# Kernel tuning notes

Hardware: AMD Instinct MI355X
Metric: run time of the kernel (lower is better)

## Reference

```python
import jax, jax.numpy as jnp
import numpy as np

N_FP = 235336   # n_fingerprint
N_WORD = 7844   # n_word
D = 10          # embed / hidden dim (hard-coded in module)
K = 23          # conv kernel 2*11+1
PAD = 11
N_ATOMS = 4096
L_WORDS = 65536


def setup_inputs() -> dict:
    key = jax.random.key(0)
    ks = jax.random.split(key, 16)
    s = 0.1  # weight init scale
    return {
        "fingerprints": jax.random.randint(ks[0], (N_ATOMS,), 0, N_FP),
        # scale adjacency so x + A@hs stays O(1) over 3 layers
        "adjacency": jax.random.uniform(ks[1], (N_ATOMS, N_ATOMS), dtype=jnp.float32) * (1.0 / N_ATOMS),
        "words": jax.random.randint(ks[2], (L_WORDS,), 0, N_WORD),
        "embed_fp": jax.random.normal(ks[3], (N_FP, D), dtype=jnp.float32) * s,
        "embed_word": jax.random.normal(ks[4], (N_WORD, D), dtype=jnp.float32) * s,
        "W_gnn_w": jax.random.normal(ks[5], (3, D, D), dtype=jnp.float32) * s,
        "W_gnn_b": jax.random.normal(ks[6], (3, D), dtype=jnp.float32) * s,
        "W_cnn_w": jax.random.normal(ks[7], (3, 1, 1, K, K), dtype=jnp.float32) * (s / K),
        "W_cnn_b": jax.random.normal(ks[8], (3,), dtype=jnp.float32) * s,
        "W_att_w": jax.random.normal(ks[9], (D, D), dtype=jnp.float32) * s,
        "W_att_b": jax.random.normal(ks[10], (D,), dtype=jnp.float32) * s,
        "W_out_w": jax.random.normal(ks[11], (3, 2 * D, 2 * D), dtype=jnp.float32) * s,
        "W_out_b": jax.random.normal(ks[12], (3, 2 * D), dtype=jnp.float32) * s,
        "W_int_w": jax.random.normal(ks[13], (2, 2 * D), dtype=jnp.float32) * s,
        "W_int_b": jax.random.normal(ks[14], (2,), dtype=jnp.float32) * s,
    }


def reference(fingerprints, adjacency, words, embed_fp, embed_word,
              W_gnn_w, W_gnn_b, W_cnn_w, W_cnn_b, W_att_w, W_att_b,
              W_out_w, W_out_b, W_int_w, W_int_b):
    # ---- Compound vector with GNN ----
    xs = embed_fp[fingerprints]                       # [N, D]
    for i in range(3):                                # fixed 3 layers
        hs = jax.nn.relu(xs @ W_gnn_w[i].T + W_gnn_b[i])
        xs = xs + adjacency @ hs                      # dense message passing
    compound = jnp.mean(xs, axis=0, keepdims=True)    # [1, D]

    # ---- Protein vector with attention-CNN ----
    ws = embed_word[words]                            # [L, D]
    t = ws[None, None]                                # [1,1,L,D] NCHW
    for i in range(3):
        t = jax.nn.relu(
            jax.lax.conv_general_dilated(t, W_cnn_w[i], (1, 1),
                                          [(PAD, PAD), (PAD, PAD)])
            + W_cnn_b[i])
    xs_p = t[0, 0]                                    # [L, D]

    h = jax.nn.relu(compound @ W_att_w.T + W_att_b)   # [1, D]
    hs_p = jax.nn.relu(xs_p @ W_att_w.T + W_att_b)    # [L, D]
    weights = jnp.tanh(h @ hs_p.T)                    # [1, L]
    ys = weights.T * hs_p                             # [L, D]
    protein = jnp.mean(ys, axis=0, keepdims=True)     # [1, D]

    # ---- Fusion MLP ----
    cat = jnp.concatenate([compound, protein], axis=1)  # [1, 2D]
    for j in range(3):
        cat = jax.nn.relu(cat @ W_out_w[j].T + W_out_b[j])
    return cat @ W_int_w.T + W_int_b                  # [1, 2]
```

## Files before the change

### kernel.cpp

```cpp
#include <hip/hip_runtime.h>
#include <hip/hip_bf16.h>
#include <math.h>

#define N_ATOMS 4096
#define L_WORDS 65536
#define DD 10
#define HALO 11

__global__ __launch_bounds__(256) void gnn_embed(
    const int* __restrict__ fp, const float* __restrict__ embed_fp,
    const float* __restrict__ Wg0, const float* __restrict__ bg0,
    float* __restrict__ xs0, float* __restrict__ hsT0)
{
    int n = blockIdx.x * blockDim.x + threadIdx.x;
    if (n >= N_ATOMS) return;
    float x[DD];
    const float* e = embed_fp + (size_t)fp[n] * DD;
    #pragma unroll
    for (int d = 0; d < DD; ++d) { x[d] = e[d]; xs0[n * DD + d] = x[d]; }
    #pragma unroll
    for (int d = 0; d < DD; ++d) {
        float v = bg0[d];
        #pragma unroll
        for (int k = 0; k < DD; ++k) v += Wg0[d * DD + k] * x[k];
        hsT0[d * N_ATOMS + n] = fmaxf(v, 0.f);
    }
}

#define GP_BLOCK 256
#define GP_RPW 4
#define GP_ROWS_BLK 16
#define GP_QCOLS 1024
#define CONV_BLOCKS 256
#define CONV_BLOCK 256

__global__ __launch_bounds__(256, 4) void fused_layer(
    const float* __restrict__ A,
    const float* __restrict__ hsT_in,
    float* __restrict__ part,
    const float* __restrict__ tin,
    const int* __restrict__ words,
    const float* __restrict__ embed_word,
    const float* __restrict__ w,
    const float* __restrict__ bptr,
    float* __restrict__ tout)
{
    __shared__ float sh[DD * GP_QCOLS];
    const int tid = threadIdx.x;

    if (blockIdx.x < CONV_BLOCKS) {
        float* s = sh;
        const int l0 = blockIdx.x * CONV_BLOCK;

        for (int idx = tid; idx < (CONV_BLOCK + 2 * HALO) * DD; idx += CONV_BLOCK) {
            int rr = idx / DD, d = idx - rr * DD;
            int gr = l0 - HALO + rr;
            float v = 0.f;
            if (gr >= 0 && gr < L_WORDS) {
                if (tin) v = tin[(size_t)gr * DD + d];
                else     v = embed_word[(size_t)words[gr] * DD + d];
            }
            s[rr * 11 + d] = v;
        }
        __syncthreads();

        const float bias = *bptr;
        float acc[DD];
        #pragma unroll
        for (int d = 0; d < DD; ++d) acc[d] = bias;

        for (int i = 0; i < 23; ++i) {
            float row[DD];
            const float* sr = &s[(tid + i) * 11];
            #pragma unroll
            for (int c = 0; c < DD; ++c) row[c] = sr[c];
            #pragma unroll
            for (int d = 0; d < DD; ++d) {
                #pragma unroll
                for (int c = 0; c < DD; ++c)
                    acc[d] += row[c] * w[i * 23 + (c - d + 11)];
            }
        }
        const int l = l0 + tid;
        #pragma unroll
        for (int d = 0; d < DD; ++d)
            tout[(size_t)l * DD + d] = fmaxf(acc[d], 0.f);
    } else {
        const int b = blockIdx.x - CONV_BLOCKS;
        const int wave = tid >> 6, lane = tid & 63;
        const int q = b & 3, rg = b >> 2;
        const int qbase = q * GP_QCOLS;

        {
            const float4* src = (const float4*)(hsT_in + qbase);
            float4* dst = (float4*)sh;
            #pragma unroll
            for (int k = 0; k < DD; ++k)
                dst[k * 256 + tid] = src[k * (N_ATOMS / 4) + tid];
        }
        __syncthreads();

        const int r0 = rg * GP_ROWS_BLK + wave * GP_RPW;
        const float4* Ar[GP_RPW];
        #pragma unroll
        for (int r = 0; r < GP_RPW; ++r)
            Ar[r] = (const float4*)(A + (size_t)(r0 + r) * N_ATOMS + qbase);
        const float4* sh4 = (const float4*)sh;

        float acc[GP_RPW][DD];
        #pragma unroll
        for (int r = 0; r < GP_RPW; ++r)
            #pragma unroll
            for (int d = 0; d < DD; ++d) acc[r][d] = 0.f;

        #pragma unroll
        for (int it = 0; it < GP_QCOLS / 256; ++it) {
            const int cb = it * 64 + lane;
            float4 a[GP_RPW];
            #pragma unroll
            for (int r = 0; r < GP_RPW; ++r) a[r] = Ar[r][cb];
            #pragma unroll
            for (int d = 0; d < DD; ++d) {
                float4 h = sh4[d * 256 + cb];
                #pragma unroll
                for (int r = 0; r < GP_RPW; ++r) {
                    acc[r][d] += a[r].x * h.x;
                    acc[r][d] += a[r].y * h.y;
                    acc[r][d] += a[r].z * h.z;
                    acc[r][d] += a[r].w * h.w;
                }
            }
        }

        #pragma unroll
        for (int m = 32; m >= 1; m >>= 1) {
            #pragma unroll
            for (int r = 0; r < GP_RPW; ++r)
                #pragma unroll
                for (int d = 0; d < DD; ++d)
                    acc[r][d] += __shfl_xor(acc[r][d], m, 64);
        }

        if (lane == 0) {
            #pragma unroll
            for (int r = 0; r < GP_RPW; ++r)
                #pragma unroll
                for (int d = 0; d < DD; ++d)
                    part[((size_t)q * N_ATOMS + r0 + r) * DD + d] = acc[r][d];
        }
    }
}

__global__ __launch_bounds__(256) void gnn_combine(
    const float* __restrict__ xs_in,
    const float* __restrict__ part,
    float* __restrict__ xs_out,
    float* __restrict__ hsT_out,
    const float* __restrict__ Wg,
    const float* __restrict__ bg,
    float* __restrict__ comp_part)
{
    const int tid = threadIdx.x, wave = tid >> 6, lane = tid & 63;
    const int n = blockIdx.x * 256 + tid;

    float x[DD];
    #pragma unroll
    for (int d = 0; d < DD; ++d) {
        float v = xs_in[n * DD + d];
        #pragma unroll
        for (int q = 0; q < 4; ++q)
            v += part[((size_t)q * N_ATOMS + n) * DD + d];
        x[d] = v;
        xs_out[n * DD + d] = v;
    }
    if (hsT_out) {
        #pragma unroll
        for (int d = 0; d < DD; ++d) {
            float v = bg[d];
            #pragma unroll
            for (int k = 0; k < DD; ++k) v += Wg[d * DD + k] * x[k];
            hsT_out[(size_t)d * N_ATOMS + n] = fmaxf(v, 0.f);
        }
    }
    if (comp_part) {
        #pragma unroll
        for (int m = 32; m >= 1; m >>= 1) {
            #pragma unroll
            for (int d = 0; d < DD; ++d) x[d] += __shfl_xor(x[d], m, 64);
        }
        __shared__ float s[4][DD];
        if (lane == 0) {
            #pragma unroll
            for (int d = 0; d < DD; ++d) s[wave][d] = x[d];
        }
        __syncthreads();
        if (tid < DD)
            comp_part[blockIdx.x * DD + tid] =
                s[0][tid] + s[1][tid] + s[2][tid] + s[3][tid];
    }
}

__global__ __launch_bounds__(256) void reduce_comp(
    const float* __restrict__ part, int npart, float* __restrict__ comp)
{
    const int tid = threadIdx.x, wave = tid >> 6, lane = tid & 63;
    float v[DD];
    #pragma unroll
    for (int d = 0; d < DD; ++d) v[d] = 0.f;
    for (int p = tid; p < npart; p += 256) {
        #pragma unroll
        for (int d = 0; d < DD; ++d) v[d] += part[p * DD + d];
    }
    #pragma unroll
    for (int off = 32; off >= 1; off >>= 1) {
        #pragma unroll
        for (int d = 0; d < DD; ++d) v[d] += __shfl_down(v[d], off, 64);
    }
    __shared__ float s[4][DD];
    if (lane == 0) {
        #pragma unroll
        for (int d = 0; d < DD; ++d) s[wave][d] = v[d];
    }
    __syncthreads();
    if (tid < DD)
        comp[tid] = (s[0][tid] + s[1][tid] + s[2][tid] + s[3][tid]) * (1.f / N_ATOMS);
}

__global__ __launch_bounds__(1024) void attention_pool(
    const float* __restrict__ xs_p,
    const float* __restrict__ comp,
    const float* __restrict__ Wa, const float* __restrict__ ba,
    float* __restrict__ att_part)
{
    const int tid = threadIdx.x, wave = tid >> 6, lane = tid & 63;
    const int l = blockIdx.x * 1024 + tid;

    float h[DD];
    #pragma unroll
    for (int d = 0; d < DD; ++d) {
        float v = ba[d];
        #pragma unroll
        for (int k = 0; k < DD; ++k) v += Wa[d * DD + k] * comp[k];
        h[d] = fmaxf(v, 0.f);
    }

    float row[DD];
    #pragma unroll
    for (int d = 0; d < DD; ++d) row[d] = xs_p[(size_t)l * DD + d];

    float hp[DD], dotv = 0.f;
    #pragma unroll
    for (int d = 0; d < DD; ++d) {
        float v = ba[d];
        #pragma unroll
        for (int k = 0; k < DD; ++k) v += Wa[d * DD + k] * row[k];
        hp[d] = fmaxf(v, 0.f);
        dotv += h[d] * hp[d];
    }
    const float wgt = tanhf(dotv);

    float y[DD];
    #pragma unroll
    for (int d = 0; d < DD; ++d) y[d] = wgt * hp[d];

    #pragma unroll
    for (int off = 32; off >= 1; off >>= 1) {
        #pragma unroll
        for (int d = 0; d < DD; ++d) y[d] += __shfl_down(y[d], off, 64);
    }
    __shared__ float s[16][DD];
    if (lane == 0) {
        #pragma unroll
        for (int d = 0; d < DD; ++d) s[wave][d] = y[d];
    }
    __syncthreads();
    if (tid < DD) {
        float v = 0.f;
        #pragma unroll
        for (int wv = 0; wv < 16; ++wv) v += s[wv][tid];
        att_part[blockIdx.x * DD + tid] = v;
    }
}

__global__ __launch_bounds__(64) void final_mlp(
    const float* __restrict__ comp,
    const float* __restrict__ att_part,
    const float* __restrict__ Wo, const float* __restrict__ bo,
    const float* __restrict__ Wi, const float* __restrict__ bi,
    float* __restrict__ out)
{
    const int t = threadIdx.x;
    float a[DD];
    #pragma unroll
    for (int d = 0; d < DD; ++d) a[d] = att_part[t * DD + d];
    #pragma unroll
    for (int off = 32; off >= 1; off >>= 1) {
        #pragma unroll
        for (int d = 0; d < DD; ++d) a[d] += __shfl_down(a[d], off, 64);
    }

    __shared__ float cat[20];
    if (t < DD) cat[t] = comp[t];
    if (t == 0) {
        #pragma unroll
        for (int d = 0; d < DD; ++d) cat[DD + d] = a[d] * (1.f / L_WORDS);
    }
    __syncthreads();

    for (int j = 0; j < 3; ++j) {
        float v = 0.f;
        if (t < 20) {
            v = bo[j * 20 + t];
            for (int k = 0; k < 20; ++k) v += Wo[j * 400 + t * 20 + k] * cat[k];
        }
        __syncthreads();
        if (t < 20) cat[t] = fmaxf(v, 0.f);
        __syncthreads();
    }
    if (t < 2) {
        float v = bi[t];
        for (int k = 0; k < 20; ++k) v += Wi[t * 20 + k] * cat[k];
        out[t] = v;
    }
}

extern "C" void kernel_launch(void* const* d_in, const int* in_sizes, int n_in,
                              void* d_out, int out_size, void* d_ws, size_t ws_size,
                              hipStream_t stream)
{
    const int*   fp     = (const int*)d_in[0];
    const float* A      = (const float*)d_in[1];
    const int*   words  = (const int*)d_in[2];
    const float* emb_fp = (const float*)d_in[3];
    const float* emb_w  = (const float*)d_in[4];
    const float* Wg     = (const float*)d_in[5];
    const float* bg     = (const float*)d_in[6];
    const float* Wc     = (const float*)d_in[7];
    const float* bc     = (const float*)d_in[8];
    const float* Wa     = (const float*)d_in[9];
    const float* ba     = (const float*)d_in[10];
    const float* Wo     = (const float*)d_in[11];
    const float* bo     = (const float*)d_in[12];
    const float* Wi     = (const float*)d_in[13];
    const float* bi     = (const float*)d_in[14];
    float* out = (float*)d_out;
    float* ws  = (float*)d_ws;

    float* xs0  = ws;
    float* xs1  = ws + 40960;
    float* hsT0 = ws + 81920;
    float* hsT1 = ws + 122880;
    float* t0   = ws + 163840;
    float* t1   = ws + 163840 + 655360;
    float* comp = ws + 163840 + 2 * 655360;
    float* part = comp + 16;
    float* comp_part = part + 163840;
    float* att_part  = comp_part + 256;

    const int fused_grid = CONV_BLOCKS + (N_ATOMS / GP_ROWS_BLK) * 4;

    gnn_embed<<<N_ATOMS / 256, 256, 0, stream>>>(fp, emb_fp, Wg, bg, xs0, hsT0);

    fused_layer<<<fused_grid, 256, 0, stream>>>(
        A, hsT0, part, nullptr, words, emb_w, Wc, bc, t0);
    gnn_combine<<<N_ATOMS / 256, 256, 0, stream>>>(
        xs0, part, xs1, hsT1, Wg + 100, bg + 10, nullptr);

    fused_layer<<<fused_grid, 256, 0, stream>>>(
        A, hsT1, part, t0, nullptr, nullptr, Wc + 529, bc + 1, t1);
    gnn_combine<<<N_ATOMS / 256, 256, 0, stream>>>(
        xs1, part, xs0, hsT0, Wg + 200, bg + 20, nullptr);

    fused_layer<<<fused_grid, 256, 0, stream>>>(
        A, hsT0, part, t1, nullptr, nullptr, Wc + 1058, bc + 2, t0);
    gnn_combine<<<N_ATOMS / 256, 256, 0, stream>>>(
        xs0, part, xs1, nullptr, nullptr, nullptr, comp_part);
    reduce_comp<<<1, 256, 0, stream>>>(comp_part, 16, comp);

    attention_pool<<<L_WORDS / 1024, 1024, 0, stream>>>(t0, comp, Wa, ba, att_part);
    final_mlp<<<1, 64, 0, stream>>>(comp, att_part, Wo, bo, Wi, bi, out);
}
```

Before: 233.6 us.

## Fuse whole pipeline into one cooperative persistent kernel with grid syncs

Replaces the sequence of about eleven kernel launches (embed, three fused GNN+conv layers, combines, reductions, attention, MLP) with a single cooperatively launched persistent kernel of 768 blocks that separates phases with grid-wide syncs. The adjacency matmul is also re-split into eight 512-column slices, which halves the shared memory per block so three blocks fit per CU, and the combine step sums eight partials. This is meant to remove launch gaps and tail effects between the many small dependent stages. In exchange it adds eight grid barriers, and it falls back to the old multi-kernel path if the cooperative launch fails.

Result: slower. 909.5 us (+289.4%).

```diff
diff --git a/kernel.cpp b/kernel.cpp
--- a/kernel.cpp
+++ b/kernel.cpp
@@ -1,49 +1,395 @@
 #include <hip/hip_runtime.h>
 #include <hip/hip_bf16.h>
+#include <hip/hip_cooperative_groups.h>
 #include <math.h>
+
+namespace cg = cooperative_groups;
 
 #define N_ATOMS 4096
 #define L_WORDS 65536
 #define DD 10
 #define HALO 11
 
-__global__ __launch_bounds__(256) void gnn_embed(
-    const int* __restrict__ fp, const float* __restrict__ embed_fp,
-    const float* __restrict__ Wg0, const float* __restrict__ bg0,
-    float* __restrict__ xs0, float* __restrict__ hsT0)
-{
-    int n = blockIdx.x * blockDim.x + threadIdx.x;
-    if (n >= N_ATOMS) return;
-    float x[DD];
-    const float* e = embed_fp + (size_t)fp[n] * DD;
-    #pragma unroll
-    for (int d = 0; d < DD; ++d) { x[d] = e[d]; xs0[n * DD + d] = x[d]; }
-    #pragma unroll
-    for (int d = 0; d < DD; ++d) {
-        float v = bg0[d];
-        #pragma unroll
-        for (int k = 0; k < DD; ++k) v += Wg0[d * DD + k] * x[k];
-        hsT0[d * N_ATOMS + n] = fmaxf(v, 0.f);
-    }
-}
-
-#define GP_BLOCK 256
+#define MG_GRID 768
+#define MG_BLOCK 256
+#define MG_QC 512
+#define MG_NQ 8
+#define MG_RPB 16
+#define MG_NRG (N_ATOMS / MG_RPB)
+#define MG_NGNN (MG_NQ * MG_NRG)
+#define MG_NCONV 256
+#define MG_NU (MG_NCONV + MG_NGNN)
+
+struct MegaArgs {
+    const int* fp; const float* A; const int* words;
+    const float* emb_fp; const float* emb_w;
+    const float* Wg; const float* bg; const float* Wc; const float* bc;
+    const float* Wa; const float* ba; const float* Wo; const float* bo;
+    const float* Wi; const float* bi;
+    float* out;
+    float* xs0; float* xs1; float* hsT0; float* hsT1;
+    float* ta; float* tb; float* part; float* comp_part; float* att_part;
+};
+
+__device__ __forceinline__ void mg_gnn_unit(
+    int g, const float* __restrict__ A, const float* __restrict__ hsT_in,
+    float* __restrict__ part, float* sh)
+{
+    const int tid = threadIdx.x, wave = tid >> 6, lane = tid & 63;
+    const int q = g & (MG_NQ - 1), rg = g >> 3;
+    const int qb4 = q * (MG_QC / 4);
+
+    {
+        const float4* src = (const float4*)hsT_in;
+        float4* dst = (float4*)sh;
+        #pragma unroll
+        for (int k = 0; k < 5; ++k) {
+            int idx = k * 256 + tid;
+            int row = idx >> 7, col = idx & 127;
+            dst[row * 128 + col] = src[(size_t)row * (N_ATOMS / 4) + qb4 + col];
+        }
+    }
+    __syncthreads();
+
+    const int r0 = rg * MG_RPB + wave * 4;
+    const float4* Ar = (const float4*)(A + (size_t)r0 * N_ATOMS) + qb4;
+    const float4* sh4 = (const float4*)sh;
+
+    float acc[4][DD];
+    #pragma unroll
+    for (int r = 0; r < 4; ++r)
+        #pragma unroll
+        for (int d = 0; d < DD; ++d) acc[r][d] = 0.f;
+
+    #pragma unroll
+    for (int it = 0; it < 2; ++it) {
+        const int cb = it * 64 + lane;
+        float4 a0 = Ar[cb];
+        float4 a1 = Ar[1024 + cb];
+        float4 a2 = Ar[2048 + cb];
+        float4 a3 = Ar[3072 + cb];
+        #pragma unroll
+        for (int d = 0; d < DD; ++d) {
+            float4 h = sh4[d * 128 + cb];
+            acc[0][d] += a0.x*h.x + a0.y*h.y + a0.z*h.z + a0.w*h.w;
+            acc[1][d] += a1.x*h.x + a1.y*h.y + a1.z*h.z + a1.w*h.w;
+            acc[2][d] += a2.x*h.x + a2.y*h.y + a2.z*h.z + a2.w*h.w;
+            acc[3][d] += a3.x*h.x + a3.y*h.y + a3.z*h.z + a3.w*h.w;
+        }
+    }
+
+    #pragma unroll
+    for (int m = 32; m >= 1; m >>= 1) {
+        #pragma unroll
+        for (int r = 0; r < 4; ++r)
+            #pragma unroll
+            for (int d = 0; d < DD; ++d)
+                acc[r][d] += __shfl_xor(acc[r][d], m, 64);
+    }
+    if (lane == 0) {
+        #pragma unroll
+        for (int r = 0; r < 4; ++r)
+            #pragma unroll
+            for (int d = 0; d < DD; ++d)
+                part[((size_t)q * N_ATOMS + r0 + r) * DD + d] = acc[r][d];
+    }
+    __syncthreads();
+}
+
+__device__ __forceinline__ void mg_conv_unit(
+    int c, const float* __restrict__ tin, const int* __restrict__ words,
+    const float* __restrict__ emb_w, const float* __restrict__ w,
+    const float* __restrict__ bptr, float* __restrict__ tout, float* sh)
+{
+    const int tid = threadIdx.x;
+    const int l0 = c * 256;
+
+    for (int idx = tid; idx < (256 + 2 * HALO) * DD; idx += 256) {
+        int rr = idx / DD, d = idx - rr * DD;
+        int gr = l0 - HALO + rr;
+        float v = 0.f;
+        if (gr >= 0 && gr < L_WORDS) {
+            if (tin) v = tin[(size_t)gr * DD + d];
+            else     v = emb_w[(size_t)words[gr] * DD + d];
+        }
+        sh[rr * 11 + d] = v;
+    }
+    __syncthreads();
+
+    const float bias = *bptr;
+    float acc[DD];
+    #pragma unroll
+    for (int d = 0; d < DD; ++d) acc[d] = bias;
+
+    for (int i = 0; i < 23; ++i) {
+        float row[DD];
+        const float* sr = &sh[(tid + i) * 11];
+        #pragma unroll
+        for (int cc = 0; cc < DD; ++cc) row[cc] = sr[cc];
+        #pragma unroll
+        for (int d = 0; d < DD; ++d) {
+            #pragma unroll
+            for (int cc = 0; cc < DD; ++cc)
+                acc[d] += row[cc] * w[i * 23 + (cc - d + 11)];
+        }
+    }
+    const int l = l0 + tid;
+    #pragma unroll
+    for (int d = 0; d < DD; ++d)
+        tout[(size_t)l * DD + d] = fmaxf(acc[d], 0.f);
+    __syncthreads();
+}
+
+__device__ __forceinline__ void mg_phaseA(
+    int layer, const float* A, const float* hsT_in, float* part,
+    const float* tin, const int* words, const float* emb_w,
+    const float* Wc, const float* bc, float* tout, float* sh)
+{
+    for (int u = blockIdx.x; u < MG_NU; u += MG_GRID) {
+        if (u < MG_NCONV)
+            mg_conv_unit(u, tin, words, emb_w, Wc + 529 * layer, bc + layer,
+                         tout, sh);
+        else
+            mg_gnn_unit(u - MG_NCONV, A, hsT_in, part, sh);
+    }
+}
+
+__device__ __forceinline__ void mg_combine(
+    const float* xs_in, const float* part, float* xs_out, float* hsT_out,
+    const float* Wg, const float* bg, float* comp_part, float* sh)
+{
+    if (blockIdx.x < 16) {
+        const int tid = threadIdx.x, wave = tid >> 6, lane = tid & 63;
+        const int n = blockIdx.x * 256 + tid;
+        float x[DD];
+        #pragma unroll
+        for (int d = 0; d < DD; ++d) {
+            float v = xs_in[n * DD + d];
+            #pragma unroll
+            for (int q = 0; q < MG_NQ; ++q)
+                v += part[((size_t)q * N_ATOMS + n) * DD + d];
+            x[d] = v;
+        }
+        if (xs_out) {
+            #pragma unroll
+            for (int d = 0; d < DD; ++d) xs_out[n * DD + d] = x[d];
+        }
+        if (hsT_out) {
+            #pragma unroll
+            for (int d = 0; d < DD; ++d) {
+                float v = bg[d];
+                #pragma unroll
+                for (int k = 0; k < DD; ++k) v += Wg[d * DD + k] * x[k];
+                hsT_out[(size_t)d * N_ATOMS + n] = fmaxf(v, 0.f);
+            }
+        }
+        if (comp_part) {
+            #pragma unroll
+            for (int m = 32; m >= 1; m >>= 1) {
+                #pragma unroll
+                for (int d = 0; d < DD; ++d) x[d] += __shfl_xor(x[d], m, 64);
+            }
+            if (lane == 0) {
+                #pragma unroll
+                for (int d = 0; d < DD; ++d) sh[wave * DD + d] = x[d];
+            }
+            __syncthreads();
+            if (tid < DD)
+                comp_part[blockIdx.x * DD + tid] =
+                    sh[tid] + sh[DD + tid] + sh[2 * DD + tid] + sh[3 * DD + tid];
+        }
+    }
+}
+
+__device__ __forceinline__ void mg_att(
+    const float* xs_p, const float* comp_part,
+    const float* Wa, const float* ba, float* att_part, float* sh)
+{
+    if (blockIdx.x < 256) {
+        const int tid = threadIdx.x, wave = tid >> 6, lane = tid & 63;
+        if (tid < DD) {
+            float c = 0.f;
+            #pragma unroll
+            for (int p = 0; p < 16; ++p) c += comp_part[p * DD + tid];
+            sh[tid] = c * (1.f / N_ATOMS);
+        }
+        __syncthreads();
+        float compv[DD];
+        #pragma unroll
+        for (int d = 0; d < DD; ++d) compv[d] = sh[d];
+
+        float h[DD];
+        #pragma unroll
+        for (int d = 0; d < DD; ++d) {
+            float v = ba[d];
+            #pragma unroll
+            for (int k = 0; k < DD; ++k) v += Wa[d * DD + k] * compv[k];
+            h[d] = fmaxf(v, 0.f);
+        }
+
+        const int l = blockIdx.x * 256 + tid;
+        float row[DD];
+        #pragma unroll
+        for (int d = 0; d < DD; ++d) row[d] = xs_p[(size_t)l * DD + d];
+
+        float hp[DD], dotv = 0.f;
+        #pragma unroll
+        for (int d = 0; d < DD; ++d) {
+            float v = ba[d];
+            #pragma unroll
+            for (int k = 0; k < DD; ++k) v += Wa[d * DD + k] * row[k];
+            hp[d] = fmaxf(v, 0.f);
+            dotv += h[d] * hp[d];
+        }
+        const float wgt = tanhf(dotv);
+
+        float y[DD];
+        #pragma unroll
+        for (int d = 0; d < DD; ++d) y[d] = wgt * hp[d];
+        #pragma unroll
+        for (int m = 32; m >= 1; m >>= 1) {
+            #pragma unroll
+            for (int d = 0; d < DD; ++d) y[d] += __shfl_xor(y[d], m, 64);
+        }
+        __syncthreads();
+        if (lane == 0) {
+            #pragma unroll
+            for (int d = 0; d < DD; ++d) sh[wave * DD + d] = y[d];
+        }
+        __syncthreads();
+        if (tid < DD)
+            att_part[blockIdx.x * DD + tid] =
+                sh[tid] + sh[DD + tid] + sh[2 * DD + tid] + sh[3 * DD + tid];
+    }
+}
+
+__device__ __forceinline__ void mg_fin(
+    const float* att_part, const float* comp_part,
+    const float* Wo, const float* bo, const float* Wi, const float* bi,
+    float* out, float* sh)
+{
+    if (blockIdx.x == 0) {
+        const int tid = threadIdx.x, wave = tid >> 6, lane = tid & 63;
+        float v[DD];
+        #pragma unroll
+        for (int d = 0; d < DD; ++d) v[d] = att_part[tid * DD + d];
+        #pragma unroll
+        for (int m = 32; m >= 1; m >>= 1) {
+            #pragma unroll
+            for (int d = 0; d < DD; ++d) v[d] += __shfl_xor(v[d], m, 64);
+        }
+        if (lane == 0) {
+            #pragma unroll
+            for (int d = 0; d < DD; ++d) sh[32 + wave * DD + d] = v[d];
+        }
+        __syncthreads();
+        if (tid < DD) {
+            float c = 0.f;
+            #pragma unroll
+            for (int p = 0; p < 16; ++p) c += comp_part[p * DD + tid];
+            sh[tid] = c * (1.f / N_ATOMS);
+            float pr = sh[32 + tid] + sh[32 + DD + tid]
+                     + sh[32 + 2 * DD + tid] + sh[32 + 3 * DD + tid];
+            sh[DD + tid] = pr * (1.f / L_WORDS);
+        }
+        __syncthreads();
+        for (int j = 0; j < 3; ++j) {
+            float vv = 0.f;
+            if (tid < 20) {
+                vv = bo[j * 20 + tid];
+                for (int k = 0; k < 20; ++k)
+                    vv += Wo[j * 400 + tid * 20 + k] * sh[k];
+            }
+            __syncthreads();
+            if (tid < 20) sh[tid] = fmaxf(vv, 0.f);
+            __syncthreads();
+        }
+        if (tid < 2) {
+            float vv = bi[tid];
+            for (int k = 0; k < 20; ++k) vv += Wi[tid * 20 + k] * sh[k];
+            out[tid] = vv;
+        }
+    }
+}
+
+__global__ __launch_bounds__(MG_BLOCK, 3) void mega(MegaArgs a)
+{
+    __shared__ float sh[DD * MG_QC];
+    cg::grid_group grid = cg::this_grid();
+    const int tid = threadIdx.x;
+
+    if (blockIdx.x < 16) {
+        const int n = blockIdx.x * 256 + tid;
+        float x[DD];
+        const float* e = a.emb_fp + (size_t)a.fp[n] * DD;
+        #pragma unroll
+        for (int d = 0; d < DD; ++d) { x[d] = e[d]; a.xs0[n * DD + d] = x[d]; }
+        #pragma unroll
+        for (int d = 0; d < DD; ++d) {
+            float v = a.bg[d];
+            #pragma unroll
+            for (int k = 0; k < DD; ++k) v += a.Wg[d * DD + k] * x[k];
+            a.hsT0[(size_t)d * N_ATOMS + n] = fmaxf(v, 0.f);
+        }
+    }
+    grid.sync();
+
+    mg_phaseA(0, a.A, a.hsT0, a.part, nullptr, a.words, a.emb_w, a.Wc, a.bc,
+              a.ta, sh);
+    grid.sync();
+    mg_combine(a.xs0, a.part, a.xs1, a.hsT1, a.Wg + 100, a.bg + 10, nullptr, sh);
+    grid.sync();
+
+    mg_phaseA(1, a.A, a.hsT1, a.part, a.ta, a.words, a.emb_w, a.Wc, a.bc,
+              a.tb, sh);
+    grid.sync();
+    mg_combine(a.xs1, a.part, a.xs0, a.hsT0, a.Wg + 200, a.bg + 20, nullptr, sh);
+    grid.sync();
+
+    mg_phaseA(2, a.A, a.hsT0, a.part, a.tb, a.words, a.emb_w, a.Wc, a.bc,
+              a.ta, sh);
+    grid.sync();
+    mg_combine(a.xs0, a.part, nullptr, nullptr, nullptr, nullptr,
+               a.comp_part, sh);
+    grid.sync();
+
+    mg_att(a.ta, a.comp_part, a.Wa, a.ba, a.att_part, sh);
+    grid.sync();
+    mg_fin(a.att_part, a.comp_part, a.Wo, a.bo, a.Wi, a.bi, a.out, sh);
+}
+
 #define GP_RPW 4
 #define GP_ROWS_BLK 16
 #define GP_QCOLS 1024
 #define CONV_BLOCKS 256
 #define CONV_BLOCK 256
 
+__global__ __launch_bounds__(256) void gnn_embed(
+    const int* __restrict__ fp, const float* __restrict__ embed_fp,
+    const float* __restrict__ Wg0, const float* __restrict__ bg0,
+    float* __restrict__ xs0, float* __restrict__ hsT0)
+{
+    int n = blockIdx.x * blockDim.x + threadIdx.x;
+    if (n >= N_ATOMS) return;
+    float x[DD];
+    const float* e = embed_fp + (size_t)fp[n] * DD;
+    #pragma unroll
+    for (int d = 0; d < DD; ++d) { x[d] = e[d]; xs0[n * DD + d] = x[d]; }
+    #pragma unroll
+    for (int d = 0; d < DD; ++d) {
+        float v = bg0[d];
+        #pragma unroll
+        for (int k = 0; k < DD; ++k) v += Wg0[d * DD + k] * x[k];
+        hsT0[d * N_ATOMS + n] = fmaxf(v, 0.f);
+    }
+}
+
 __global__ __launch_bounds__(256, 4) void fused_layer(
-    const float* __restrict__ A,
-    const float* __restrict__ hsT_in,
+    const float* __restrict__ A, const float* __restrict__ hsT_in,
     float* __restrict__ part,
-    const float* __restrict__ tin,
-    const int* __restrict__ words,
-    const float* __restrict__ embed_word,
-    const float* __restrict__ w,
-    const float* __restrict__ bptr,
-    float* __restrict__ tout)
+    const float* __restrict__ tin, const int* __restrict__ words,
+    const float* __restrict__ embed_word, const float* __restrict__ w,
+    const float* __restrict__ bptr, float* __restrict__ tout)
 {
     __shared__ float sh[DD * GP_QCOLS];
     const int tid = threadIdx.x;
@@ -51,7 +397,6 @@
     if (blockIdx.x < CONV_BLOCKS) {
         float* s = sh;
         const int l0 = blockIdx.x * CONV_BLOCK;
-
         for (int idx = tid; idx < (CONV_BLOCK + 2 * HALO) * DD; idx += CONV_BLOCK) {
             int rr = idx / DD, d = idx - rr * DD;
             int gr = l0 - HALO + rr;
@@ -63,12 +408,10 @@
             s[rr * 11 + d] = v;
         }
         __syncthreads();
-
         const float bias = *bptr;
         float acc[DD];
         #pragma unroll
         for (int d = 0; d < DD; ++d) acc[d] = bias;
-
         for (int i = 0; i < 23; ++i) {
             float row[DD];
             const float* sr = &s[(tid + i) * 11];
@@ -90,7 +433,6 @@
         const int wave = tid >> 6, lane = tid & 63;
         const int q = b & 3, rg = b >> 2;
         const int qbase = q * GP_QCOLS;
-
         {
             const float4* src = (const float4*)(hsT_in + qbase);
             float4* dst = (float4*)sh;
@@ -99,39 +441,35 @@
                 dst[k * 256 + tid] = src[k * (N_ATOMS / 4) + tid];
         }
         __syncthreads();
-
         const int r0 = rg * GP_ROWS_BLK + wave * GP_RPW;
         const float4* Ar[GP_RPW];
         #pragma unroll
         for (int r = 0; r < GP_RPW; ++r)
             Ar[r] = (const float4*)(A + (size_t)(r0 + r) * N_ATOMS + qbase);
         const float4* sh4 = (const float4*)sh;
-
         float acc[GP_RPW][DD];
         #pragma unroll
         for (int r = 0; r < GP_RPW; ++r)
             #pragma unroll
             for (int d = 0; d < DD; ++d) acc[r][d] = 0.f;
-
         #pragma unroll
         for (int it = 0; it < GP_QCOLS / 256; ++it) {
             const int cb = it * 64 + lane;
-            float4 a[GP_RPW];
-            #pragma unroll
-            for (int r = 0; r < GP_RPW; ++r) a[r] = Ar[r][cb];
+            float4 av[GP_RPW];
+            #pragma unroll
+            for (int r = 0; r < GP_RPW; ++r) av[r] = Ar[r][cb];
             #pragma unroll
             for (int d = 0; d < DD; ++d) {
                 float4 h = sh4[d * 256 + cb];
                 #pragma unroll
                 for (int r = 0; r < GP_RPW; ++r) {
-                    acc[r][d] += a[r].x * h.x;
-                    acc[r][d] += a[r].y * h.y;
-                    acc[r][d] += a[r].z * h.z;
-                    acc[r][d] += a[r].w * h.w;
+                    acc[r][d] += av[r].x * h.x;
+                    acc[r][d] += av[r].y * h.y;
+                    acc[r][d] += av[r].z * h.z;
+                    acc[r][d] += av[r].w * h.w;
                 }
             }
         }
-
         #pragma unroll
         for (int m = 32; m >= 1; m >>= 1) {
             #pragma unroll
@@ -140,7 +478,6 @@
                 for (int d = 0; d < DD; ++d)
                     acc[r][d] += __shfl_xor(acc[r][d], m, 64);
         }
-
         if (lane == 0) {
             #pragma unroll
             for (int r = 0; r < GP_RPW; ++r)
@@ -152,17 +489,13 @@
 }
 
 __global__ __launch_bounds__(256) void gnn_combine(
-    const float* __restrict__ xs_in,
-    const float* __restrict__ part,
-    float* __restrict__ xs_out,
-    float* __restrict__ hsT_out,
-    const float* __restrict__ Wg,
-    const float* __restrict__ bg,
+    const float* __restrict__ xs_in, const float* __restrict__ part,
+    float* __restrict__ xs_out, float* __restrict__ hsT_out,
+    const float* __restrict__ Wg, const float* __restrict__ bg,
     float* __restrict__ comp_part)
 {
     const int tid = threadIdx.x, wave = tid >> 6, lane = tid & 63;
     const int n = blockIdx.x * 256 + tid;
-
     float x[DD];
     #pragma unroll
     for (int d = 0; d < DD; ++d) {
@@ -227,14 +560,12 @@
 }
 
 __global__ __launch_bounds__(1024) void attention_pool(
-    const float* __restrict__ xs_p,
-    const float* __restrict__ comp,
+    const float* __restrict__ xs_p, const float* __restrict__ comp,
     const float* __restrict__ Wa, const float* __restrict__ ba,
     float* __restrict__ att_part)
 {
     const int tid = threadIdx.x, wave = tid >> 6, lane = tid & 63;
     const int l = blockIdx.x * 1024 + tid;
-
     float h[DD];
     #pragma unroll
     for (int d = 0; d < DD; ++d) {
@@ -243,11 +574,9 @@
         for (int k = 0; k < DD; ++k) v += Wa[d * DD + k] * comp[k];
         h[d] = fmaxf(v, 0.f);
     }
-
     float row[DD];
     #pragma unroll
     for (int d = 0; d < DD; ++d) row[d] = xs_p[(size_t)l * DD + d];
-
     float hp[DD], dotv = 0.f;
     #pragma unroll
     for (int d = 0; d < DD; ++d) {
@@ -258,11 +587,9 @@
         dotv += h[d] * hp[d];
     }
     const float wgt = tanhf(dotv);
-
     float y[DD];
     #pragma unroll
     for (int d = 0; d < DD; ++d) y[d] = wgt * hp[d];
-
     #pragma unroll
     for (int off = 32; off >= 1; off >>= 1) {
         #pragma unroll
@@ -283,8 +610,7 @@
 }
 
 __global__ __launch_bounds__(64) void final_mlp(
-    const float* __restrict__ comp,
-    const float* __restrict__ att_part,
+    const float* __restrict__ comp, const float* __restrict__ att_part,
     const float* __restrict__ Wo, const float* __restrict__ bo,
     const float* __restrict__ Wi, const float* __restrict__ bi,
     float* __restrict__ out)
@@ -298,7 +624,6 @@
         #pragma unroll
         for (int d = 0; d < DD; ++d) a[d] += __shfl_down(a[d], off, 64);
     }
-
     __shared__ float cat[20];
     if (t < DD) cat[t] = comp[t];
     if (t == 0) {
@@ -306,7 +631,6 @@
         for (int d = 0; d < DD; ++d) cat[DD + d] = a[d] * (1.f / L_WORDS);
     }
     __syncthreads();
-
     for (int j = 0; j < 3; ++j) {
         float v = 0.f;
         if (t < 20) {
@@ -350,33 +674,38 @@
     float* xs1  = ws + 40960;
     float* hsT0 = ws + 81920;
     float* hsT1 = ws + 122880;
-    float* t0   = ws + 163840;
-    float* t1   = ws + 163840 + 655360;
-    float* comp = ws + 163840 + 2 * 655360;
-    float* part = comp + 16;
-    float* comp_part = part + 163840;
-    float* att_part  = comp_part + 256;
-
-    const int fused_grid = CONV_BLOCKS + (N_ATOMS / GP_ROWS_BLK) * 4;
-
-    gnn_embed<<<N_ATOMS / 256, 256, 0, stream>>>(fp, emb_fp, Wg, bg, xs0, hsT0);
-
-    fused_layer<<<fused_grid, 256, 0, stream>>>(
-        A, hsT0, part, nullptr, words, emb_w, Wc, bc, t0);
-    gnn_combine<<<N_ATOMS / 256, 256, 0, stream>>>(
-        xs0, part, xs1, hsT1, Wg + 100, bg + 10, nullptr);
-
-    fused_layer<<<fused_grid, 256, 0, stream>>>(
-        A, hsT1, part, t0, nullptr, nullptr, Wc + 529, bc + 1, t1);
-    gnn_combine<<<N_ATOMS / 256, 256, 0, stream>>>(
-        xs1, part, xs0, hsT0, Wg + 200, bg + 20, nullptr);
-
-    fused_layer<<<fused_grid, 256, 0, stream>>>(
-        A, hsT0, part, t1, nullptr, nullptr, Wc + 1058, bc + 2, t0);
-    gnn_combine<<<N_ATOMS / 256, 256, 0, stream>>>(
-        xs0, part, xs1, nullptr, nullptr, nullptr, comp_part);
-    reduce_comp<<<1, 256, 0, stream>>>(comp_part, 16, comp);
-
-    attention_pool<<<L_WORDS / 1024, 1024, 0, stream>>>(t0, comp, Wa, ba, att_part);
-    final_mlp<<<1, 64, 0, stream>>>(comp, att_part, Wo, bo, Wi, bi, out);
-}
+    float* ta   = ws + 163840;
+    float* tb   = ws + 819200;
+    float* part = ws + 1474560;
+    float* comp_part = ws + 1802240;
+    float* att_part  = ws + 1802496;
+    float* comp      = ws + 1805056;
+
+    MegaArgs ma = { fp, A, words, emb_fp, emb_w, Wg, bg, Wc, bc,
+                    Wa, ba, Wo, bo, Wi, bi, out,
+                    xs0, xs1, hsT0, hsT1, ta, tb, part, comp_part, att_part };
+    void* kp[1] = { &ma };
+    hipError_t err = hipLaunchCooperativeKernel(
+        (void*)mega, dim3(MG_GRID), dim3(MG_BLOCK), kp, 0, stream);
+
+    if (err != hipSuccess) {
+        (void)hipGetLastError();
+        const int fused_grid = CONV_BLOCKS + (N_ATOMS / GP_ROWS_BLK) * 4;
+        gnn_embed<<<N_ATOMS / 256, 256, 0, stream>>>(fp, emb_fp, Wg, bg, xs0, hsT0);
+        fused_layer<<<fused_grid, 256, 0, stream>>>(
+            A, hsT0, part, nullptr, words, emb_w, Wc, bc, ta);
+        gnn_combine<<<N_ATOMS / 256, 256, 0, stream>>>(
+            xs0, part, xs1, hsT1, Wg + 100, bg + 10, nullptr);
+        fused_layer<<<fused_grid, 256, 0, stream>>>(
+            A, hsT1, part, ta, nullptr, nullptr, Wc + 529, bc + 1, tb);
+        gnn_combine<<<N_ATOMS / 256, 256, 0, stream>>>(
+            xs1, part, xs0, hsT0, Wg + 200, bg + 20, nullptr);
+        fused_layer<<<fused_grid, 256, 0, stream>>>(
+            A, hsT0, part, tb, nullptr, nullptr, Wc + 1058, bc + 2, ta);
+        gnn_combine<<<N_ATOMS / 256, 256, 0, stream>>>(
+            xs0, part, xs1, nullptr, nullptr, nullptr, comp_part);
+        reduce_comp<<<1, 256, 0, stream>>>(comp_part, 16, comp);
+        attention_pool<<<L_WORDS / 1024, 1024, 0, stream>>>(ta, comp, Wa, ba, att_part);
+        final_mlp<<<1, 64, 0, stream>>>(comp, att_part, Wo, bo, Wi, bi, out);
+    }
+}
```

## Fuse GNN combine and final reductions into producer kernels via last-block atomics

Applied to the files above, without the earlier changes.

Removes the separate gnn_combine, reduce_comp and final_mlp launches. The last of the four column-quarter blocks for each row group (detected with an atomic counter) does the combine, the next-layer hidden projection and the compound partial sums, and a second counter lets the last block produce the compound mean. The attention kernel likewise uses a last-block counter to run the final MLP. Counters are zeroed inside the embed kernel. This cuts launch overhead and inter-kernel gaps in exchange for extra threadfences and atomics, plus a serial tail in the last block.

New measurement: 769.9 us. +229.6%, slower.

```diff
diff --git a/kernel.cpp b/kernel.cpp
--- a/kernel.cpp
+++ b/kernel.cpp
@@ -7,51 +7,59 @@
 #define DD 10
 #define HALO 11
 
-__global__ __launch_bounds__(256) void gnn_embed(
-    const int* __restrict__ fp, const float* __restrict__ embed_fp,
-    const float* __restrict__ Wg0, const float* __restrict__ bg0,
-    float* __restrict__ xs0, float* __restrict__ hsT0)
-{
-    int n = blockIdx.x * blockDim.x + threadIdx.x;
-    if (n >= N_ATOMS) return;
-    float x[DD];
-    const float* e = embed_fp + (size_t)fp[n] * DD;
-    #pragma unroll
-    for (int d = 0; d < DD; ++d) { x[d] = e[d]; xs0[n * DD + d] = x[d]; }
-    #pragma unroll
-    for (int d = 0; d < DD; ++d) {
-        float v = bg0[d];
-        #pragma unroll
-        for (int k = 0; k < DD; ++k) v += Wg0[d * DD + k] * x[k];
-        hsT0[d * N_ATOMS + n] = fmaxf(v, 0.f);
-    }
-}
-
-#define GP_BLOCK 256
 #define GP_RPW 4
 #define GP_ROWS_BLK 16
 #define GP_QCOLS 1024
 #define CONV_BLOCKS 256
 #define CONV_BLOCK 256
+#define N_RG (N_ATOMS / GP_ROWS_BLK)
+
+__global__ __launch_bounds__(256) void gnn_embed(
+    const int* __restrict__ fp, const float* __restrict__ embed_fp,
+    const float* __restrict__ Wg0, const float* __restrict__ bg0,
+    float* __restrict__ xs0, float* __restrict__ hsT0,
+    int* __restrict__ cnts)
+{
+    const int tid = threadIdx.x;
+    if (blockIdx.x == 0) {
+        for (int i = tid; i < 3 * N_RG + 2; i += 256) cnts[i] = 0;
+    }
+    int n = blockIdx.x * blockDim.x + tid;
+    if (n >= N_ATOMS) return;
+    float x[DD];
+    const float* e = embed_fp + (size_t)fp[n] * DD;
+    #pragma unroll
+    for (int d = 0; d < DD; ++d) { x[d] = e[d]; xs0[n * DD + d] = x[d]; }
+    #pragma unroll
+    for (int d = 0; d < DD; ++d) {
+        float v = bg0[d];
+        #pragma unroll
+        for (int k = 0; k < DD; ++k) v += Wg0[d * DD + k] * x[k];
+        hsT0[d * N_ATOMS + n] = fmaxf(v, 0.f);
+    }
+}
 
 __global__ __launch_bounds__(256, 4) void fused_layer(
-    const float* __restrict__ A,
-    const float* __restrict__ hsT_in,
+    const float* __restrict__ A, const float* __restrict__ hsT_in,
     float* __restrict__ part,
-    const float* __restrict__ tin,
-    const int* __restrict__ words,
-    const float* __restrict__ embed_word,
-    const float* __restrict__ w,
-    const float* __restrict__ bptr,
-    float* __restrict__ tout)
+    const float* __restrict__ xs_in, float* __restrict__ xs_out,
+    float* __restrict__ hsT_out,
+    const float* __restrict__ Wg, const float* __restrict__ bg,
+    float* __restrict__ comp_part,
+    float* __restrict__ comp,
+    int* __restrict__ cnt,
+    int* __restrict__ comp_cnt,
+    const float* __restrict__ tin, const int* __restrict__ words,
+    const float* __restrict__ embed_word, const float* __restrict__ w,
+    const float* __restrict__ bptr, float* __restrict__ tout)
 {
     __shared__ float sh[DD * GP_QCOLS];
+    __shared__ int s_last, s_last2;
     const int tid = threadIdx.x;
 
     if (blockIdx.x < CONV_BLOCKS) {
         float* s = sh;
         const int l0 = blockIdx.x * CONV_BLOCK;
-
         for (int idx = tid; idx < (CONV_BLOCK + 2 * HALO) * DD; idx += CONV_BLOCK) {
             int rr = idx / DD, d = idx - rr * DD;
             int gr = l0 - HALO + rr;
@@ -68,7 +76,6 @@
         float acc[DD];
         #pragma unroll
         for (int d = 0; d < DD; ++d) acc[d] = bias;
-
         for (int i = 0; i < 23; ++i) {
             float row[DD];
             const float* sr = &s[(tid + i) * 11];
@@ -116,18 +123,18 @@
         #pragma unroll
         for (int it = 0; it < GP_QCOLS / 256; ++it) {
             const int cb = it * 64 + lane;
-            float4 a[GP_RPW];
-            #pragma unroll
-            for (int r = 0; r < GP_RPW; ++r) a[r] = Ar[r][cb];
+            float4 av[GP_RPW];
+            #pragma unroll
+            for (int r = 0; r < GP_RPW; ++r) av[r] = Ar[r][cb];
             #pragma unroll
             for (int d = 0; d < DD; ++d) {
                 float4 h = sh4[d * 256 + cb];
                 #pragma unroll
                 for (int r = 0; r < GP_RPW; ++r) {
-                    acc[r][d] += a[r].x * h.x;
-                    acc[r][d] += a[r].y * h.y;
-                    acc[r][d] += a[r].z * h.z;
-                    acc[r][d] += a[r].w * h.w;
+                    acc[r][d] += av[r].x * h.x;
+                    acc[r][d] += av[r].y * h.y;
+                    acc[r][d] += av[r].z * h.z;
+                    acc[r][d] += av[r].w * h.w;
                 }
             }
         }
@@ -140,187 +147,158 @@
                 for (int d = 0; d < DD; ++d)
                     acc[r][d] += __shfl_xor(acc[r][d], m, 64);
         }
-
         if (lane == 0) {
             #pragma unroll
             for (int r = 0; r < GP_RPW; ++r)
                 #pragma unroll
                 for (int d = 0; d < DD; ++d)
                     part[((size_t)q * N_ATOMS + r0 + r) * DD + d] = acc[r][d];
+            __threadfence();
+        }
+        __syncthreads();
+        if (tid == 0) s_last = (atomicAdd(&cnt[rg], 1) == 3);
+        __syncthreads();
+
+        if (s_last) {
+            __threadfence();
+            if (tid < GP_ROWS_BLK * DD) {
+                const int row = tid / DD, d = tid - row * DD;
+                const int n = rg * GP_ROWS_BLK + row;
+                float v = xs_in[n * DD + d];
+                #pragma unroll
+                for (int qq = 0; qq < 4; ++qq)
+                    v += part[((size_t)qq * N_ATOMS + n) * DD + d];
+                if (xs_out) xs_out[n * DD + d] = v;
+                sh[row * DD + d] = v;
+            }
+            __syncthreads();
+            if (hsT_out && tid < DD * GP_ROWS_BLK) {
+                const int d = tid >> 4, n0 = tid & 15;
+                float v = bg[d];
+                #pragma unroll
+                for (int k = 0; k < DD; ++k) v += Wg[d * DD + k] * sh[n0 * DD + k];
+                hsT_out[(size_t)d * N_ATOMS + rg * GP_ROWS_BLK + n0] = fmaxf(v, 0.f);
+            }
+            if (comp_part) {
+                if (tid < DD) {
+                    float s = 0.f;
+                    #pragma unroll
+                    for (int row = 0; row < GP_ROWS_BLK; ++row) s += sh[row * DD + tid];
+                    comp_part[rg * DD + tid] = s;
+                }
+                __threadfence();
+                __syncthreads();
+                if (tid == 0) s_last2 = (atomicAdd(comp_cnt, 1) == N_RG - 1);
+                __syncthreads();
+                if (s_last2) {
+                    __threadfence();
+                    if (tid < DD) {
+                        float s = 0.f;
+                        for (int p = 0; p < N_RG; ++p) s += comp_part[p * DD + tid];
+                        comp[tid] = s * (1.f / N_ATOMS);
+                    }
+                }
+            }
         }
     }
 }
 
-__global__ __launch_bounds__(256) void gnn_combine(
-    const float* __restrict__ xs_in,
-    const float* __restrict__ part,
-    float* __restrict__ xs_out,
-    float* __restrict__ hsT_out,
-    const float* __restrict__ Wg,
-    const float* __restrict__ bg,
-    float* __restrict__ comp_part)
-{
-    const int tid = threadIdx.x, wave = tid >> 6, lane = tid & 63;
-    const int n = blockIdx.x * 256 + tid;
-
-    float x[DD];
-    #pragma unroll
-    for (int d = 0; d < DD; ++d) {
-        float v = xs_in[n * DD + d];
-        #pragma unroll
-        for (int q = 0; q < 4; ++q)
-            v += part[((size_t)q * N_ATOMS + n) * DD + d];
-        x[d] = v;
-        xs_out[n * DD + d] = v;
-    }
-    if (hsT_out) {
-        #pragma unroll
-        for (int d = 0; d < DD; ++d) {
-            float v = bg[d];
-            #pragma unroll
-            for (int k = 0; k < DD; ++k) v += Wg[d * DD + k] * x[k];
-            hsT_out[(size_t)d * N_ATOMS + n] = fmaxf(v, 0.f);
-        }
-    }
-    if (comp_part) {
-        #pragma unroll
-        for (int m = 32; m >= 1; m >>= 1) {
-            #pragma unroll
-            for (int d = 0; d < DD; ++d) x[d] += __shfl_xor(x[d], m, 64);
-        }
-        __shared__ float s[4][DD];
-        if (lane == 0) {
-            #pragma unroll
-            for (int d = 0; d < DD; ++d) s[wave][d] = x[d];
-        }
-        __syncthreads();
-        if (tid < DD)
-            comp_part[blockIdx.x * DD + tid] =
-                s[0][tid] + s[1][tid] + s[2][tid] + s[3][tid];
-    }
-}
-
-__global__ __launch_bounds__(256) void reduce_comp(
-    const float* __restrict__ part, int npart, float* __restrict__ comp)
-{
-    const int tid = threadIdx.x, wave = tid >> 6, lane = tid & 63;
-    float v[DD];
-    #pragma unroll
-    for (int d = 0; d < DD; ++d) v[d] = 0.f;
-    for (int p = tid; p < npart; p += 256) {
-        #pragma unroll
-        for (int d = 0; d < DD; ++d) v[d] += part[p * DD + d];
-    }
-    #pragma unroll
-    for (int off = 32; off >= 1; off >>= 1) {
-        #pragma unroll
-        for (int d = 0; d < DD; ++d) v[d] += __shfl_down(v[d], off, 64);
-    }
-    __shared__ float s[4][DD];
-    if (lane == 0) {
-        #pragma unroll
-        for (int d = 0; d < DD; ++d) s[wave][d] = v[d];
-    }
-    __syncthreads();
-    if (tid < DD)
-        comp[tid] = (s[0][tid] + s[1][tid] + s[2][tid] + s[3][tid]) * (1.f / N_ATOMS);
-}
-
-__global__ __launch_bounds__(1024) void attention_pool(
-    const float* __restrict__ xs_p,
-    const float* __restrict__ comp,
+__global__ __launch_bounds__(1024) void attention_fin(
+    const float* __restrict__ xs_p, const float* __restrict__ comp,
     const float* __restrict__ Wa, const float* __restrict__ ba,
-    float* __restrict__ att_part)
-{
-    const int tid = threadIdx.x, wave = tid >> 6, lane = tid & 63;
-    const int l = blockIdx.x * 1024 + tid;
-
-    float h[DD];
-    #pragma unroll
-    for (int d = 0; d < DD; ++d) {
-        float v = ba[d];
-        #pragma unroll
-        for (int k = 0; k < DD; ++k) v += Wa[d * DD + k] * comp[k];
-        h[d] = fmaxf(v, 0.f);
-    }
-
-    float row[DD];
-    #pragma unroll
-    for (int d = 0; d < DD; ++d) row[d] = xs_p[(size_t)l * DD + d];
-
-    float hp[DD], dotv = 0.f;
-    #pragma unroll
-    for (int d = 0; d < DD; ++d) {
-        float v = ba[d];
-        #pragma unroll
-        for (int k = 0; k < DD; ++k) v += Wa[d * DD + k] * row[k];
-        hp[d] = fmaxf(v, 0.f);
-        dotv += h[d] * hp[d];
-    }
-    const float wgt = tanhf(dotv);
-
-    float y[DD];
-    #pragma unroll
-    for (int d = 0; d < DD; ++d) y[d] = wgt * hp[d];
-
-    #pragma unroll
-    for (int off = 32; off >= 1; off >>= 1) {
-        #pragma unroll
-        for (int d = 0; d < DD; ++d) y[d] += __shfl_down(y[d], off, 64);
-    }
-    __shared__ float s[16][DD];
-    if (lane == 0) {
-        #pragma unroll
-        for (int d = 0; d < DD; ++d) s[wave][d] = y[d];
-    }
-    __syncthreads();
-    if (tid < DD) {
-        float v = 0.f;
-        #pragma unroll
-        for (int wv = 0; wv < 16; ++wv) v += s[wv][tid];
-        att_part[blockIdx.x * DD + tid] = v;
-    }
-}
-
-__global__ __launch_bounds__(64) void final_mlp(
-    const float* __restrict__ comp,
-    const float* __restrict__ att_part,
+    float* __restrict__ att_part, int* __restrict__ att_cnt,
     const float* __restrict__ Wo, const float* __restrict__ bo,
     const float* __restrict__ Wi, const float* __restrict__ bi,
     float* __restrict__ out)
 {
-    const int t = threadIdx.x;
-    float a[DD];
-    #pragma unroll
-    for (int d = 0; d < DD; ++d) a[d] = att_part[t * DD + d];
-    #pragma unroll
-    for (int off = 32; off >= 1; off >>= 1) {
-        #pragma unroll
-        for (int d = 0; d < DD; ++d) a[d] += __shfl_down(a[d], off, 64);
-    }
-
-    __shared__ float cat[20];
-    if (t < DD) cat[t] = comp[t];
-    if (t == 0) {
-        #pragma unroll
-        for (int d = 0; d < DD; ++d) cat[DD + d] = a[d] * (1.f / L_WORDS);
+    __shared__ float s[16][DD];
+    __shared__ float cat[32];
+    __shared__ int s_last;
+    const int tid = threadIdx.x, wave = tid >> 6, lane = tid & 63;
+    const int l = blockIdx.x * 1024 + tid;
+
+    float h[DD];
+    #pragma unroll
+    for (int d = 0; d < DD; ++d) {
+        float v = ba[d];
+        #pragma unroll
+        for (int k = 0; k < DD; ++k) v += Wa[d * DD + k] * comp[k];
+        h[d] = fmaxf(v, 0.f);
+    }
+
+    float row[DD];
+    #pragma unroll
+    for (int d = 0; d < DD; ++d) row[d] = xs_p[(size_t)l * DD + d];
+
+    float hp[DD], dotv = 0.f;
+    #pragma unroll
+    for (int d = 0; d < DD; ++d) {
+        float v = ba[d];
+        #pragma unroll
+        for (int k = 0; k < DD; ++k) v += Wa[d * DD + k] * row[k];
+        hp[d] = fmaxf(v, 0.f);
+        dotv += h[d] * hp[d];
+    }
+    const float wgt = tanhf(dotv);
+
+    float y[DD];
+    #pragma unroll
+    for (int d = 0; d < DD; ++d) y[d] = wgt * hp[d];
+    #pragma unroll
+    for (int m = 32; m >= 1; m >>= 1) {
+        #pragma unroll
+        for (int d = 0; d < DD; ++d) y[d] += __shfl_xor(y[d], m, 64);
+    }
+    if (lane == 0) {
+        #pragma unroll
+        for (int d = 0; d < DD; ++d) s[wave][d] = y[d];
     }
     __syncthreads();
-
-    for (int j = 0; j < 3; ++j) {
+    if (tid < DD) {
         float v = 0.f;
-        if (t < 20) {
-            v = bo[j * 20 + t];
-            for (int k = 0; k < 20; ++k) v += Wo[j * 400 + t * 20 + k] * cat[k];
-        }
-        __syncthreads();
-        if (t < 20) cat[t] = fmaxf(v, 0.f);
-        __syncthreads();
-    }
-    if (t < 2) {
-        float v = bi[t];
-        for (int k = 0; k < 20; ++k) v += Wi[t * 20 + k] * cat[k];
-        out[t] = v;
+        #pragma unroll
+        for (int wv = 0; wv < 16; ++wv) v += s[wv][tid];
+        att_part[blockIdx.x * DD + tid] = v;
+    }
+    __threadfence();
+    __syncthreads();
+    if (tid == 0) s_last = (atomicAdd(att_cnt, 1) == (L_WORDS / 1024) - 1);
+    __syncthreads();
+
+    if (s_last) {
+        __threadfence();
+        if (tid < 64) {
+            float a[DD];
+            #pragma unroll
+            for (int d = 0; d < DD; ++d) a[d] = att_part[tid * DD + d];
+            #pragma unroll
+            for (int m = 32; m >= 1; m >>= 1) {
+                #pragma unroll
+                for (int d = 0; d < DD; ++d) a[d] += __shfl_xor(a[d], m, 64);
+            }
+            if (tid == 0) {
+                #pragma unroll
+                for (int d = 0; d < DD; ++d)
+                    cat[DD + d] = a[d] * (1.f / L_WORDS);
+            }
+        }
+        if (tid < DD) cat[tid] = comp[tid];
+        __syncthreads();
+        for (int j = 0; j < 3; ++j) {
+            float v = 0.f;
+            if (tid < 20) {
+                v = bo[j * 20 + tid];
+                for (int k = 0; k < 20; ++k) v += Wo[j * 400 + tid * 20 + k] * cat[k];
+            }
+            __syncthreads();
+            if (tid < 20) cat[tid] = fmaxf(v, 0.f);
+            __syncthreads();
+        }
+        if (tid < 2) {
+            float v = bi[tid];
+            for (int k = 0; k < 20; ++k) v += Wi[tid * 20 + k] * cat[k];
+            out[tid] = v;
+        }
     }
 }
 
@@ -350,33 +328,36 @@
     float* xs1  = ws + 40960;
     float* hsT0 = ws + 81920;
     float* hsT1 = ws + 122880;
-    float* t0   = ws + 163840;
-    float* t1   = ws + 163840 + 655360;
-    float* comp = ws + 163840 + 2 * 655360;
-    float* part = comp + 16;
-    float* comp_part = part + 163840;
-    float* att_part  = comp_part + 256;
-
-    const int fused_grid = CONV_BLOCKS + (N_ATOMS / GP_ROWS_BLK) * 4;
-
-    gnn_embed<<<N_ATOMS / 256, 256, 0, stream>>>(fp, emb_fp, Wg, bg, xs0, hsT0);
+    float* ta   = ws + 163840;
+    float* tb   = ws + 819200;
+    float* part = ws + 1474560;
+    float* comp_part = ws + 1638400;
+    float* att_part  = ws + 1640960;
+    float* comp      = ws + 1641600;
+    int*   cnts      = (int*)(ws + 1641616);
+    int*   comp_cnt  = cnts + 3 * N_RG;
+    int*   att_cnt   = comp_cnt + 1;
+
+    const int fused_grid = CONV_BLOCKS + N_RG * 4;
+
+    gnn_embed<<<N_ATOMS / 256, 256, 0, stream>>>(
+        fp, emb_fp, Wg, bg, xs0, hsT0, cnts);
 
     fused_layer<<<fused_grid, 256, 0, stream>>>(
-        A, hsT0, part, nullptr, words, emb_w, Wc, bc, t0);
-    gnn_combine<<<N_ATOMS / 256, 256, 0, stream>>>(
-        xs0, part, xs1, hsT1, Wg + 100, bg + 10, nullptr);
+        A, hsT0, part, xs0, xs1, hsT1, Wg + 100, bg + 10,
+        nullptr, nullptr, cnts + 0 * N_RG, comp_cnt,
+        nullptr, words, emb_w, Wc, bc, ta);
 
     fused_layer<<<fused_grid, 256, 0, stream>>>(
-        A, hsT1, part, t0, nullptr, nullptr, Wc + 529, bc + 1, t1);
-    gnn_combine<<<N_ATOMS / 256, 256, 0, stream>>>(
-        xs1, part, xs0, hsT0, Wg + 200, bg + 20, nullptr);
+        A, hsT1, part, xs1, xs0, hsT0, Wg + 200, bg + 20,
+        nullptr, nullptr, cnts + 1 * N_RG, comp_cnt,
+        ta, nullptr, nullptr, Wc + 529, bc + 1, tb);
 
     fused_layer<<<fused_grid, 256, 0, stream>>>(
-        A, hsT0, part, t1, nullptr, nullptr, Wc + 1058, bc + 2, t0);
-    gnn_combine<<<N_ATOMS / 256, 256, 0, stream>>>(
-        xs0, part, xs1, nullptr, nullptr, nullptr, comp_part);
-    reduce_comp<<<1, 256, 0, stream>>>(comp_part, 16, comp);
-
-    attention_pool<<<L_WORDS / 1024, 1024, 0, stream>>>(t0, comp, Wa, ba, att_part);
-    final_mlp<<<1, 64, 0, stream>>>(comp, att_part, Wo, bo, Wi, bi, out);
+        A, hsT0, part, xs0, nullptr, nullptr, nullptr, nullptr,
+        comp_part, comp, cnts + 2 * N_RG, comp_cnt,
+        tb, nullptr, nullptr, Wc + 1058, bc + 2, ta);
+
+    attention_fin<<<L_WORDS / 1024, 1024, 0, stream>>>(
+        ta, comp, Wa, ba, att_part, att_cnt, Wo, bo, Wi, bi, out);
 }
```
